# Performance work log

Hardware: AMD Instinct MI355X
Metric: run time of the kernel (lower is better)

## Reference

```python
import jax, jax.numpy as jnp
import numpy as np

B, BS, M, D = 64, 8, 512, 256  # b = bs * neg_sample_num, neg_sample_num = 8
NEG_FILL = -1e10


def setup_inputs() -> dict:
    key = jax.random.key(0)
    ks = jax.random.split(key, 7)
    x = jax.random.normal(ks[0], (B, M, D), jnp.float32)
    y = jax.random.normal(ks[1], (BS, M, D), jnp.float32)
    mask_x = jax.random.randint(ks[2], (B, M), 0, 2).astype(bool).at[:, 0].set(True)
    mask_y = jax.random.randint(ks[3], (BS, M), 0, 2).astype(bool).at[:, 0].set(True)
    scale = 1.0 / np.sqrt(D)
    Wq = jax.random.normal(ks[4], (D, D), jnp.float32) * scale  # torch Linear weight [out,in]
    Wk = jax.random.normal(ks[5], (D, D), jnp.float32) * scale
    Wv = jax.random.normal(ks[6], (D, D), jnp.float32) * scale
    return {"x": x, "y": y, "mask_x": mask_x, "mask_y": mask_y, "Wq": Wq, "Wk": Wk, "Wv": Wv}


def reference(x, y, mask_x, mask_y, Wq, Wk, Wv):
    # Projections (torch Linear: x @ W.T, no bias)
    Qx, Kx, Vx = x @ Wq.T, x @ Wk.T, x @ Wv.T
    Qy, Ky, Vy = y @ Wq.T, y @ Wk.T, y @ Wv.T
    b, m, d = Qx.shape
    bs = Ky.shape[0]
    neg = b // bs  # neg_sample_num branch (bs != b)

    scores_x = jnp.einsum('bid,bjd->bij', Qx, Kx)   # [b,m,m]
    scores_y = jnp.einsum('bid,bjd->bij', Qy, Ky)   # [bs,m,m]
    # Q_x grouped as [bs, neg, m, d] then transposed to [neg, bs, m, d];
    # K_y is tiled over neg (pure broadcast), so contract directly against [bs,m,d].
    Qx_e = Qx.reshape(bs, neg, m, d).swapaxes(0, 1)  # [neg,bs,m,d]
    scores_xy = jnp.einsum('nsid,sjd->nsij', Qx_e, Ky)  # [neg,bs,m,m]

    mx = mask_x[:, :, None]  # [b,m,1]
    my = mask_y[:, :, None]  # [bs,m,1]
    scores_x = jnp.where(mx & mx.swapaxes(1, 2), scores_x, NEG_FILL)
    scores_y = jnp.where(my & my.swapaxes(1, 2), scores_y, NEG_FILL)

    mask_xy = mask_x.reshape(bs, neg, m, 1).swapaxes(0, 1) & mask_y[None, :, None, :]  # [neg,bs,m,m]
    scores_xy = jnp.where(mask_xy, scores_xy, NEG_FILL)

    # y_len[n, s] = sum(mask_y[s]) for every n (repeat/view/sum/transpose in torch)
    y_len = jnp.broadcast_to(jnp.sum(mask_y.astype(jnp.int32), axis=1)[None, :], (neg, bs))

    probs_x = jax.nn.softmax(scores_x, axis=-1)
    probs_y = jax.nn.softmax(scores_y, axis=-1)
    probs_xy = jax.nn.softmax(scores_xy, axis=-1)

    ctx_x = jnp.einsum('bij,bjd->bid', probs_x, Vx)
    ctx_y = jnp.einsum('bij,bjd->bid', probs_y, Vy)
    return (ctx_x, ctx_y, scores_x, scores_y, probs_xy, mask_xy, y_len)
```

## Files before the change

### kernel.cpp

```cpp
#include <hip/hip_runtime.h>
#include <cstdint>

#define NEG_FILL_F (-10000000000.0f)
constexpr int BB     = 64;
constexpr int BS_    = 8;
constexpr int MM     = 512;
constexpr int DD     = 256;
constexpr int ROWS_X = BB * MM;
constexpr int ROWS_Y = BS_ * MM;
constexpr int ROWS_ALL = ROWS_X + ROWS_Y;
constexpr int K3     = 768;

typedef __attribute__((ext_vector_type(8))) short short8;
typedef __attribute__((ext_vector_type(4))) float f32x4;

__device__ inline unsigned short rne_bf16(float f) {
    unsigned int u = __float_as_uint(f);
    u = (u + 0x7FFFu + ((u >> 16) & 1u)) >> 16;
    return (unsigned short)u;
}
__device__ inline float bf2f(unsigned short h) {
    return __uint_as_float(((unsigned int)h) << 16);
}

__device__ inline f32x4 mfma16(short8 a, short8 b, f32x4 c) {
    return __builtin_amdgcn_mfma_f32_16x16x32_bf16(a, b, c, 0, 0, 0);
}

__device__ inline void gld16(const unsigned short* g, unsigned short* l) {
    __builtin_amdgcn_global_load_lds(
        (const __attribute__((address_space(1))) unsigned int*)g,
        (__attribute__((address_space(3))) unsigned int*)l, 16, 0, 0);
}

__device__ inline void mfma_4x4(const short8 af[4], const short8 bf_[4],
                                f32x4 acc[4][4]) {
    #pragma unroll
    for (int i = 0; i < 4; ++i)
        #pragma unroll
        for (int j = 0; j < 4; ++j)
            acc[i][j] = mfma16(af[i], bf_[j], acc[i][j]);
}

__device__ inline void stage768_rot(unsigned short* dstbase,
                                    const unsigned short* __restrict__ src,
                                    int ck, int wave, int lane)
{
    #pragma unroll
    for (int s = 0; s < 6; ++s) {
        const int c  = s * 256 + wave * 64 + lane;
        const int r  = c / 12;
        const int q  = c - r * 12;
        const int rm = r % 12;
        int cin = q - rm;
        cin += (cin >> 31) & 12;
        gld16(src + (size_t)r * K3 + ck * 96 + cin * 8,
              dstbase + (size_t)(s * 256 + wave * 64) * 8);
    }
}

__device__ inline void frag4_rot96(const unsigned short (*T)[96], int rbase,
                                   int lid, const int rm[4], int c0,
                                   short8 f[4])
{
    #pragma unroll
    for (int i = 0; i < 4; ++i) {
        int q = c0 + rm[i];
        if (q >= 12) q -= 12;
        f[i] = *(const short8*)&T[rbase + i * 16 + lid][q * 8];
    }
}

__global__ __launch_bounds__(256) void convw_kernel(
    const float* __restrict__ Wq, const float* __restrict__ Wk,
    const float* __restrict__ Wv, unsigned short* __restrict__ Wb)
{
    const int g  = blockIdx.x * 256 + threadIdx.x;
    const int e  = g * 8;
    const int zi = e >> 16;
    const int off = e & 65535;
    const float* W = (zi == 0) ? Wq : (zi == 1 ? Wk : Wv);
    float4 v0 = *(const float4*)(W + off);
    float4 v1 = *(const float4*)(W + off + 4);
    const float fv[8] = {v0.x, v0.y, v0.z, v0.w, v1.x, v1.y, v1.z, v1.w};
    unsigned short o[24];
    #pragma unroll
    for (int i = 0; i < 8; ++i) {
        unsigned short h = rne_bf16(fv[i]);
        unsigned short l = rne_bf16(fv[i] - bf2f(h));
        o[i*3+0] = h; o[i*3+1] = h; o[i*3+2] = l;
    }
    unsigned short* dst = Wb + (size_t)zi * 196608 + (size_t)off * 3;
    #pragma unroll
    for (int s = 0; s < 3; ++s) {
        short8 v;
        #pragma unroll
        for (int e2 = 0; e2 < 8; ++e2) v[e2] = (short)o[s*8+e2];
        *(short8*)(dst + s * 8) = v;
    }
}

__global__ __launch_bounds__(256) void convx_kernel(
    const float* __restrict__ x, const float* __restrict__ y,
    unsigned short* __restrict__ xs)
{
    const int g   = blockIdx.x * 256 + threadIdx.x;
    const int row = g >> 5;
    const int off = (g & 31) * 8;
    const float* src = (row < ROWS_X) ? (x + (size_t)row * DD)
                                      : (y + (size_t)(row - ROWS_X) * DD);
    float4 v0 = *(const float4*)(src + off);
    float4 v1 = *(const float4*)(src + off + 4);
    const float fv[8] = {v0.x, v0.y, v0.z, v0.w, v1.x, v1.y, v1.z, v1.w};
    unsigned short o[24];
    #pragma unroll
    for (int i = 0; i < 8; ++i) {
        unsigned short h = rne_bf16(fv[i]);
        unsigned short l = rne_bf16(fv[i] - bf2f(h));
        o[i*3+0] = h; o[i*3+1] = l; o[i*3+2] = h;
    }
    unsigned short* dst = xs + (size_t)row * K3 + (size_t)off * 3;
    #pragma unroll
    for (int s = 0; s < 3; ++s) {
        short8 w;
        #pragma unroll
        for (int e2 = 0; e2 < 8; ++e2) w[e2] = (short)o[s*8+e2];
        *(short8*)(dst + s * 8) = w;
    }
}

__global__ __launch_bounds__(256) void proj_kernel(
    const unsigned short* __restrict__ xs,
    const unsigned short* __restrict__ Wb,
    unsigned short* __restrict__ Qa, unsigned short* __restrict__ Kb,
    unsigned short* __restrict__ Vt,
    unsigned short* __restrict__ Qp, unsigned short* __restrict__ Kp)
{
    const int z    = blockIdx.z;
    const int row0 = blockIdx.x * 128;
    const int col0 = blockIdx.y * 128;
    const unsigned short* Asrc = xs + (size_t)row0 * K3;
    const unsigned short* Bsrc = Wb + (size_t)z * 196608 + (size_t)col0 * K3;

    __shared__ unsigned short Ab[128][96];
    __shared__ unsigned short Bb[128][96];

    const int t = threadIdx.x;
    const int wave = t >> 6, lane = t & 63, quad = lane >> 4, lid = lane & 15;
    const int wrow = (wave & 1) * 64, wcol = (wave >> 1) * 64;

    int rma[4], rmb[4];
    #pragma unroll
    for (int i = 0; i < 4; ++i) {
        rma[i] = (wrow + i * 16 + lid) % 12;
        rmb[i] = (wcol + i * 16 + lid) % 12;
    }

    f32x4 acc[4][4];
    #pragma unroll
    for (int i = 0; i < 4; ++i)
        #pragma unroll
        for (int j = 0; j < 4; ++j) acc[i][j] = (f32x4){0.f, 0.f, 0.f, 0.f};

    for (int ck = 0; ck < 8; ++ck) {
        stage768_rot(&Ab[0][0], Asrc, ck, wave, lane);
        stage768_rot(&Bb[0][0], Bsrc, ck, wave, lane);
        __syncthreads();
        #pragma unroll
        for (int kk = 0; kk < 96; kk += 32) {
            const int c0 = (kk >> 3) + quad;
            short8 af[4], bf_[4];
            frag4_rot96(Ab, wrow, lid, rma, c0, af);
            frag4_rot96(Bb, wcol, lid, rmb, c0, bf_);
            mfma_4x4(af, bf_, acc);
        }
        __syncthreads();
    }

    if (z == 2) {
        #pragma unroll
        for (int i = 0; i < 4; ++i) {
            const int rg = row0 + wrow + i * 16 + quad * 4;
            const int b  = rg >> 9;
            const int j  = rg & 511;
            #pragma unroll
            for (int jt = 0; jt < 4; ++jt) {
                const int col = col0 + wcol + jt * 16 + lid;
                *(ushort4*)(Vt + (size_t)b * DD * MM + (size_t)col * MM + j) =
                    make_ushort4(rne_bf16(acc[i][jt][0]), rne_bf16(acc[i][jt][1]),
                                 rne_bf16(acc[i][jt][2]), rne_bf16(acc[i][jt][3]));
            }
        }
    } else {
        unsigned short* dst = (z == 0) ? Qa : Kb;
        const bool aform = (z == 0);
        unsigned short* plain = nullptr;
        int rbase_plain = 0;
        if (z == 0 && row0 < ROWS_X) { plain = Qp; rbase_plain = 0; }
        if (z == 1 && row0 >= ROWS_X) { plain = Kp; rbase_plain = ROWS_X; }
        #pragma unroll
        for (int i = 0; i < 4; ++i) {
            const int rg = row0 + wrow + i * 16 + quad * 4;
            #pragma unroll
            for (int r = 0; r < 4; ++r) {
                unsigned short* rowp = dst + (size_t)(rg + r) * K3;
                unsigned short* prow = plain
                    ? (plain + (size_t)(rg + r - rbase_plain) * DD) : nullptr;
                #pragma unroll
                for (int jt = 0; jt < 4; ++jt) {
                    const int col = col0 + wcol + jt * 16 + lid;
                    const float v = acc[i][jt][r];
                    unsigned short h = rne_bf16(v);
                    unsigned short l = rne_bf16(v - bf2f(h));
                    rowp[3*col+0] = h;
                    rowp[3*col+1] = aform ? l : h;
                    rowp[3*col+2] = aform ? h : l;
                    if (prow) prow[col] = h;
                }
            }
        }
    }
}

__global__ __launch_bounds__(256) void scores_self_kernel(
    const unsigned short* __restrict__ Qa,
    const unsigned short* __restrict__ Kb,
    const int* __restrict__ mask_x, const int* __restrict__ mask_y,
    float* __restrict__ Sbase, float2* __restrict__ pstats)
{
    const int z    = blockIdx.z;
    const int row0 = blockIdx.x * 128;
    const int col0 = blockIdx.y * 128;
    const unsigned short* Asrc = Qa + (size_t)(z * MM + row0) * K3;
    const unsigned short* Bsrc = Kb + (size_t)(z * MM + col0) * K3;
    const int* msk = (z < 64) ? (mask_x + z * MM) : (mask_y + (z - 64) * MM);
    float* S = Sbase + (size_t)z * MM * MM;

    __shared__ unsigned short Ab[128][96];
    __shared__ unsigned short Bb[128][96];
    __shared__ float pm2[128][2];
    __shared__ float ps2[128][2];

    const int t = threadIdx.x;
    const int wave = t >> 6, lane = t & 63, quad = lane >> 4, lid = lane & 15;
    const int wrow = (wave & 1) * 64, wcol = (wave >> 1) * 64;

    int rma[4], rmb[4];
    #pragma unroll
    for (int i = 0; i < 4; ++i) {
        rma[i] = (wrow + i * 16 + lid) % 12;
        rmb[i] = (wcol + i * 16 + lid) % 12;
    }

    f32x4 acc[4][4];
    #pragma unroll
    for (int i = 0; i < 4; ++i)
        #pragma unroll
        for (int j = 0; j < 4; ++j) acc[i][j] = (f32x4){0.f, 0.f, 0.f, 0.f};

    for (int ck = 0; ck < 8; ++ck) {
        stage768_rot(&Ab[0][0], Asrc, ck, wave, lane);
        stage768_rot(&Bb[0][0], Bsrc, ck, wave, lane);
        __syncthreads();
        #pragma unroll
        for (int kk = 0; kk < 96; kk += 32) {
            const int c0 = (kk >> 3) + quad;
            short8 af[4], bf_[4];
            frag4_rot96(Ab, wrow, lid, rma, c0, af);
            frag4_rot96(Bb, wcol, lid, rmb, c0, bf_);
            mfma_4x4(af, bf_, acc);
        }
        __syncthreads();
    }

    int mcol[4];
    #pragma unroll
    for (int jt = 0; jt < 4; ++jt) mcol[jt] = msk[col0 + wcol + jt * 16 + lid];

    #pragma unroll
    for (int i = 0; i < 4; ++i) {
        const int rl0 = wrow + i * 16 + quad * 4;
        #pragma unroll
        for (int r = 0; r < 4; ++r) {
            const int rlocal = rl0 + r;
            const int rg = row0 + rlocal;
            const bool mr = (msk[rg] != 0);
            float* Srow = S + (size_t)rg * MM;
            float v[4];
            float mt = -3.4e38f;
            #pragma unroll
            for (int jt = 0; jt < 4; ++jt) {
                const int col = col0 + wcol + jt * 16 + lid;
                const bool valid = mr && (mcol[jt] != 0);
                v[jt] = valid ? acc[i][jt][r] : NEG_FILL_F;
                Srow[col] = v[jt];
                mt = fmaxf(mt, v[jt]);
            }
            #pragma unroll
            for (int o = 1; o < 16; o <<= 1) mt = fmaxf(mt, __shfl_xor(mt, o));
            float se = 0.f;
            #pragma unroll
            for (int jt = 0; jt < 4; ++jt) se += __expf(v[jt] - mt);
            #pragma unroll
            for (int o = 1; o < 16; o <<= 1) se += __shfl_xor(se, o);
            if (lid == 0) { pm2[rlocal][wave >> 1] = mt; ps2[rlocal][wave >> 1] = se; }
        }
    }
    __syncthreads();
    if (t < 128) {
        const float m0 = pm2[t][0], m1 = pm2[t][1];
        const float mm = fmaxf(m0, m1);
        const float ss = ps2[t][0] * __expf(m0 - mm) + ps2[t][1] * __expf(m1 - mm);
        pstats[(size_t)(z * 4 + blockIdx.y) * MM + row0 + t] = make_float2(mm, ss);
    }
}

__global__ __launch_bounds__(256) void scores_xy_kernel(
    const unsigned short* __restrict__ Qp, const unsigned short* __restrict__ Kp,
    const int* __restrict__ mask_x, const int* __restrict__ mask_y,
    float* __restrict__ Sbase, float* __restrict__ Mbase,
    float2* __restrict__ pstats)
{
    const int z = blockIdx.z;
    const int n = z >> 3, s = z & 7;
    const int bq = s * 8 + n;
    const int bk = s;
    const int row0 = blockIdx.x * 128;
    const int col0 = blockIdx.y * 128;
    const unsigned short* Asrc = Qp + (size_t)(bq * MM + row0) * DD;
    const unsigned short* Bsrc = Kp + (size_t)(bk * MM + col0) * DD;
    const int* mq = mask_x + bq * MM;
    const int* mk = mask_y + bk * MM;
    float* Sl = Sbase + (size_t)z * MM * MM;
    float* Ml = Mbase + (size_t)z * MM * MM;

    __shared__ unsigned short Ab[128][64];
    __shared__ unsigned short Bb[128][64];
    __shared__ float pm2[128][2];
    __shared__ float ps2[128][2];

    const int t = threadIdx.x;
    const int wave = t >> 6, lane = t & 63, quad = lane >> 4, lid = lane & 15;
    const int wrow = (wave & 1) * 64, wcol = (wave >> 1) * 64;
    const int x7 = lid & 7;

    f32x4 acc[4][4];
    #pragma unroll
    for (int i = 0; i < 4; ++i)
        #pragma unroll
        for (int j = 0; j < 4; ++j) acc[i][j] = (f32x4){0.f, 0.f, 0.f, 0.f};

    for (int ck = 0; ck < 4; ++ck) {
        #pragma unroll
        for (int s4 = 0; s4 < 4; ++s4) {
            const int c   = s4 * 256 + wave * 64 + lane;
            const int r   = c >> 3;
            const int cin = (c & 7) ^ (r & 7);
            gld16(Asrc + (size_t)r * DD + ck * 64 + cin * 8,
                  &Ab[0][0] + (size_t)(s4 * 256 + wave * 64) * 8);
        }
        #pragma unroll
        for (int s4 = 0; s4 < 4; ++s4) {
            const int c   = s4 * 256 + wave * 64 + lane;
            const int r   = c >> 3;
            const int cin = (c & 7) ^ (r & 7);
            gld16(Bsrc + (size_t)r * DD + ck * 64 + cin * 8,
                  &Bb[0][0] + (size_t)(s4 * 256 + wave * 64) * 8);
        }
        __syncthreads();
        #pragma unroll
        for (int kk = 0; kk < 64; kk += 32) {
            const int c0 = (kk >> 3) + quad;
            const int q  = c0 ^ x7;
            short8 af[4], bf_[4];
            #pragma unroll
            for (int i = 0; i < 4; ++i) {
                af[i]  = *(const short8*)&Ab[wrow + i * 16 + lid][q * 8];
                bf_[i] = *(const short8*)&Bb[wcol + i * 16 + lid][q * 8];
            }
            mfma_4x4(af, bf_, acc);
        }
        __syncthreads();
    }

    int mcol[4];
    #pragma unroll
    for (int jt = 0; jt < 4; ++jt) mcol[jt] = mk[col0 + wcol + jt * 16 + lid];

    #pragma unroll
    for (int i = 0; i < 4; ++i) {
        const int rl0 = wrow + i * 16 + quad * 4;
        #pragma unroll
        for (int r = 0; r < 4; ++r) {
            const int rlocal = rl0 + r;
            const int rg = row0 + rlocal;
            const bool mr = (mq[rg] != 0);
            float* Srow = Sl + (size_t)rg * MM;
            float* Mrow = Ml + (size_t)rg * MM;
            float v[4];
            float mt = -3.4e38f;
            #pragma unroll
            for (int jt = 0; jt < 4; ++jt) {
                const int col = col0 + wcol + jt * 16 + lid;
                const bool valid = mr && (mcol[jt] != 0);
                v[jt] = valid ? acc[i][jt][r] : NEG_FILL_F;
                Srow[col] = v[jt];
                Mrow[col] = valid ? 1.0f : 0.0f;
                mt = fmaxf(mt, v[jt]);
            }
            #pragma unroll
            for (int o = 1; o < 16; o <<= 1) mt = fmaxf(mt, __shfl_xor(mt, o));
            float se = 0.f;
            #pragma unroll
            for (int jt = 0; jt < 4; ++jt) se += __expf(v[jt] - mt);
            #pragma unroll
            for (int o = 1; o < 16; o <<= 1) se += __shfl_xor(se, o);
            if (lid == 0) { pm2[rlocal][wave >> 1] = mt; ps2[rlocal][wave >> 1] = se; }
        }
    }
    __syncthreads();
    if (t < 128) {
        const float m0 = pm2[t][0], m1 = pm2[t][1];
        const float mm = fmaxf(m0, m1);
        const float ss = ps2[t][0] * __expf(m0 - mm) + ps2[t][1] * __expf(m1 - mm);
        pstats[(size_t)(z * 4 + blockIdx.y) * MM + row0 + t] = make_float2(mm, ss);
    }
}

__global__ __launch_bounds__(256) void reduce4_kernel(
    const float2* __restrict__ p, float2* __restrict__ st)
{
    const int row = blockIdx.x * 256 + threadIdx.x;
    const int z = row >> 9, rl = row & 511;
    float m = -3.4e38f, s = 0.f;
    #pragma unroll
    for (int by = 0; by < 4; ++by) {
        float2 v = p[(size_t)(z * 4 + by) * MM + rl];
        float nm = fmaxf(m, v.x);
        s = s * __expf(m - nm) + v.y * __expf(v.x - nm);
        m = nm;
    }
    st[row] = make_float2(m, 1.0f / s);
}

__global__ __launch_bounds__(256) void ctx_kernel(
    const float* __restrict__ Sbase, const float2* __restrict__ stats,
    const unsigned short* __restrict__ Vt_base, float* __restrict__ Obase)
{
    const int b = blockIdx.z;
    const float*          S  = Sbase + (size_t)b * MM * MM;
    const float2*         st = stats + (size_t)b * MM;
    const unsigned short* Vt = Vt_base + (size_t)b * DD * MM;
    float*                O  = Obase + (size_t)b * MM * DD;

    const int row0 = blockIdx.x * 128;
    const int col0 = blockIdx.y * 128;

    __shared__ unsigned short Ab[128][72];
    __shared__ unsigned short Bb[128][64];

    const int t = threadIdx.x;
    const int wave = t >> 6, lane = t & 63, quad = lane >> 4, lid = lane & 15;
    const int wrow = (wave & 1) * 64, wcol = (wave >> 1) * 64;
    const int x7 = lid & 7;

    f32x4 acc[4][4];
    #pragma unroll
    for (int i = 0; i < 4; ++i)
        #pragma unroll
        for (int j = 0; j < 4; ++j) acc[i][j] = (f32x4){0.f, 0.f, 0.f, 0.f};

    for (int ck = 0; ck < 8; ++ck) {
        #pragma unroll
        for (int s4 = 0; s4 < 4; ++s4) {
            const int c   = s4 * 256 + wave * 64 + lane;
            const int r   = c >> 3;
            const int cin = (c & 7) ^ (r & 7);
            gld16(Vt + (size_t)(col0 + r) * MM + ck * 64 + cin * 8,
                  &Bb[0][0] + (size_t)(s4 * 256 + wave * 64) * 8);
        }
        #pragma unroll
        for (int s4 = 0; s4 < 4; ++s4) {
            const int c   = s4 * 256 + t;
            const int row = c >> 3;
            const int j8  = (c & 7) * 8;
            const float* sp = S + (size_t)(row0 + row) * MM + ck * 64 + j8;
            float4 v0 = *(const float4*)sp;
            float4 v1 = *(const float4*)(sp + 4);
            const float pm = st[row0 + row].x;
            short8 pk;
            pk[0] = (short)rne_bf16(__expf(v0.x - pm));
            pk[1] = (short)rne_bf16(__expf(v0.y - pm));
            pk[2] = (short)rne_bf16(__expf(v0.z - pm));
            pk[3] = (short)rne_bf16(__expf(v0.w - pm));
            pk[4] = (short)rne_bf16(__expf(v1.x - pm));
            pk[5] = (short)rne_bf16(__expf(v1.y - pm));
            pk[6] = (short)rne_bf16(__expf(v1.z - pm));
            pk[7] = (short)rne_bf16(__expf(v1.w - pm));
            *(short8*)&Ab[row][j8] = pk;
        }
        __syncthreads();
        #pragma unroll
        for (int kk = 0; kk < 64; kk += 32) {
            const int c0 = (kk >> 3) + quad;
            const int q  = c0 ^ x7;
            short8 af[4], bf_[4];
            #pragma unroll
            for (int i = 0; i < 4; ++i) {
                af[i]  = *(const short8*)&Ab[wrow + i * 16 + lid][kk + quad * 8];
                bf_[i] = *(const short8*)&Bb[wcol + i * 16 + lid][q * 8];
            }
            mfma_4x4(af, bf_, acc);
        }
        __syncthreads();
    }

    #pragma unroll
    for (int i = 0; i < 4; ++i) {
        const int rgb = row0 + wrow + i * 16 + quad * 4;
        float inv[4];
        #pragma unroll
        for (int r = 0; r < 4; ++r) inv[r] = st[rgb + r].y;
        #pragma unroll
        for (int jt = 0; jt < 4; ++jt) {
            const int col = col0 + wcol + jt * 16 + lid;
            #pragma unroll
            for (int r = 0; r < 4; ++r)
                O[(size_t)(rgb + r) * DD + col] = acc[i][jt][r] * inv[r];
        }
    }
}

__global__ __launch_bounds__(128) void softmax_apply(
    float* __restrict__ S, const float2* __restrict__ stats)
{
    const int row = blockIdx.x;
    const float2 st = stats[row];
    float4* r = (float4*)(S + (size_t)row * MM) + threadIdx.x;
    float4 v = *r;
    v.x = __expf(v.x - st.x) * st.y;
    v.y = __expf(v.y - st.x) * st.y;
    v.z = __expf(v.z - st.x) * st.y;
    v.w = __expf(v.w - st.x) * st.y;
    *r = v;
}

__global__ void ylen_kernel(const int* __restrict__ mask_y, float* __restrict__ out)
{
    const int s = blockIdx.x;
    const int lane = threadIdx.x;
    int c = 0;
    #pragma unroll
    for (int k = 0; k < 8; ++k) c += (mask_y[s * MM + k * 64 + lane] != 0);
    #pragma unroll
    for (int off = 32; off; off >>= 1) c += __shfl_xor(c, off);
    if (lane < 8) out[lane * 8 + s] = (float)c;
}

extern "C" void kernel_launch(void* const* d_in, const int* in_sizes, int n_in,
                              void* d_out, int out_size, void* d_ws, size_t ws_size,
                              hipStream_t stream)
{
    const float* x      = (const float*)d_in[0];
    const float* y      = (const float*)d_in[1];
    const int*   mask_x = (const int*)d_in[2];
    const int*   mask_y = (const int*)d_in[3];
    const float* Wq     = (const float*)d_in[4];
    const float* Wk     = (const float*)d_in[5];
    const float* Wv     = (const float*)d_in[6];
    float* out = (float*)d_out;

    unsigned short* Wb = (unsigned short*)d_ws;
    unsigned short* Qa = Wb + 589824;
    unsigned short* Kb = Qa + 28311552;
    unsigned short* Vt = Kb + 28311552;
    float2* stats_x  = (float2*)(Vt + 9437184);
    float2* stats_xy = stats_x + ROWS_ALL;
    float2* ps_x  = stats_x + (ROWS_ALL + ROWS_X);
    float2* ps_xy = ps_x + (64 + 8) * 4 * 512;

    float* out_ctx_x = out;
    float* out_sx    = out + 9437184;
    float* out_pxy   = out + 28311552;
    float* out_mxy   = out + 45088768;
    float* out_ylen  = out + 61865984;

    unsigned short* xs = (unsigned short*)out_pxy;
    unsigned short* Qp = (unsigned short*)out_ctx_x;
    unsigned short* Kp = Qp + (size_t)ROWS_X * DD;

    convw_kernel<<<96, 256, 0, stream>>>(Wq, Wk, Wv, Wb);
    convx_kernel<<<4608, 256, 0, stream>>>(x, y, xs);

    proj_kernel<<<dim3(288, 2, 3), 256, 0, stream>>>(xs, Wb, Qa, Kb, Vt, Qp, Kp);

    scores_self_kernel<<<dim3(4, 4, 72), 256, 0, stream>>>(
        Qa, Kb, mask_x, mask_y, out_sx, ps_x);
    scores_xy_kernel<<<dim3(4, 4, 64), 256, 0, stream>>>(
        Qp, Kp, mask_x, mask_y, out_pxy, out_mxy, ps_xy);

    reduce4_kernel<<<(ROWS_ALL + ROWS_X) / 256, 256, 0, stream>>>(ps_x, stats_x);

    ctx_kernel<<<dim3(4, 2, 72), 256, 0, stream>>>(out_sx, stats_x, Vt, out_ctx_x);

    softmax_apply<<<ROWS_X, 128, 0, stream>>>(out_pxy, stats_xy);

    ylen_kernel<<<8, 64, 0, stream>>>(mask_y, out_ylen);
}
```

Measured before the change: 552.4 us.

## Store Q/K as hi|lo planes, fuse input conversion into projection, drop plain copies

Replaces the interleaved 3-way split-bf16 layout (K=768) with a planar hi/lo layout (K=512 storage), so the emulated 3-term product reads hi/lo slices by offset rather than storing duplicated halves. This cuts the Q/K workspace footprint and write traffic. The x/y bf16 split conversion is fused into the projection's A-tile staging, and the separate convx kernel is removed. Plain Q/K copies for the cross scores are dropped because that kernel now reads the hi plane of Qa/Kb directly. The ctx A-tile gets an XOR swizzle instead of padding, and a few launches are reordered; the risk is extra fp32 global loads and conversion work inside the projection loop.

Measured after the change: 567.6 us. +2.8%, slower.

```diff
diff --git a/kernel.cpp b/kernel.cpp
--- a/kernel.cpp
+++ b/kernel.cpp
@@ -9,7 +9,7 @@
 constexpr int ROWS_X = BB * MM;
 constexpr int ROWS_Y = BS_ * MM;
 constexpr int ROWS_ALL = ROWS_X + ROWS_Y;
-constexpr int K3     = 768;
+constexpr int KS     = 512;
 
 typedef __attribute__((ext_vector_type(8))) short short8;
 typedef __attribute__((ext_vector_type(4))) float f32x4;
@@ -42,9 +42,10 @@
             acc[i][j] = mfma16(af[i], bf_[j], acc[i][j]);
 }
 
-__device__ inline void stage768_rot(unsigned short* dstbase,
-                                    const unsigned short* __restrict__ src,
-                                    int ck, int wave, int lane)
+template<bool ASIDE>
+__device__ inline void stage_qk(unsigned short* dstbase,
+                                const unsigned short* __restrict__ src,
+                                int ck, int wave, int lane)
 {
     #pragma unroll
     for (int s = 0; s < 6; ++s) {
@@ -54,7 +55,12 @@
         const int rm = r % 12;
         int cin = q - rm;
         cin += (cin >> 31) & 12;
-        gld16(src + (size_t)r * K3 + ck * 96 + cin * 8,
+        const int slotb = ck * 96 + cin * 8;
+        const int p  = slotb >> 8;
+        const int c8 = slotb & 255;
+        const int off = ASIDE ? ((p == 1) ? 256 : 0)
+                              : ((p == 2) ? 256 : 0);
+        gld16(src + (size_t)r * KS + off + c8,
               dstbase + (size_t)(s * 256 + wave * 64) * 8);
     }
 }
@@ -79,68 +85,35 @@
     const int e  = g * 8;
     const int zi = e >> 16;
     const int off = e & 65535;
+    const int row = off >> 8, k0 = off & 255;
     const float* W = (zi == 0) ? Wq : (zi == 1 ? Wk : Wv);
     float4 v0 = *(const float4*)(W + off);
     float4 v1 = *(const float4*)(W + off + 4);
     const float fv[8] = {v0.x, v0.y, v0.z, v0.w, v1.x, v1.y, v1.z, v1.w};
-    unsigned short o[24];
+    short8 hh, ll;
     #pragma unroll
     for (int i = 0; i < 8; ++i) {
         unsigned short h = rne_bf16(fv[i]);
-        unsigned short l = rne_bf16(fv[i] - bf2f(h));
-        o[i*3+0] = h; o[i*3+1] = h; o[i*3+2] = l;
-    }
-    unsigned short* dst = Wb + (size_t)zi * 196608 + (size_t)off * 3;
-    #pragma unroll
-    for (int s = 0; s < 3; ++s) {
-        short8 v;
-        #pragma unroll
-        for (int e2 = 0; e2 < 8; ++e2) v[e2] = (short)o[s*8+e2];
-        *(short8*)(dst + s * 8) = v;
-    }
-}
-
-__global__ __launch_bounds__(256) void convx_kernel(
+        hh[i] = (short)h;
+        ll[i] = (short)rne_bf16(fv[i] - bf2f(h));
+    }
+    unsigned short* dst = Wb + (size_t)zi * 131072 + (size_t)row * KS;
+    *(short8*)(dst + k0)       = hh;
+    *(short8*)(dst + 256 + k0) = ll;
+}
+
+__global__ __launch_bounds__(256) void proj_kernel(
     const float* __restrict__ x, const float* __restrict__ y,
-    unsigned short* __restrict__ xs)
-{
-    const int g   = blockIdx.x * 256 + threadIdx.x;
-    const int row = g >> 5;
-    const int off = (g & 31) * 8;
-    const float* src = (row < ROWS_X) ? (x + (size_t)row * DD)
-                                      : (y + (size_t)(row - ROWS_X) * DD);
-    float4 v0 = *(const float4*)(src + off);
-    float4 v1 = *(const float4*)(src + off + 4);
-    const float fv[8] = {v0.x, v0.y, v0.z, v0.w, v1.x, v1.y, v1.z, v1.w};
-    unsigned short o[24];
-    #pragma unroll
-    for (int i = 0; i < 8; ++i) {
-        unsigned short h = rne_bf16(fv[i]);
-        unsigned short l = rne_bf16(fv[i] - bf2f(h));
-        o[i*3+0] = h; o[i*3+1] = l; o[i*3+2] = h;
-    }
-    unsigned short* dst = xs + (size_t)row * K3 + (size_t)off * 3;
-    #pragma unroll
-    for (int s = 0; s < 3; ++s) {
-        short8 w;
-        #pragma unroll
-        for (int e2 = 0; e2 < 8; ++e2) w[e2] = (short)o[s*8+e2];
-        *(short8*)(dst + s * 8) = w;
-    }
-}
-
-__global__ __launch_bounds__(256) void proj_kernel(
-    const unsigned short* __restrict__ xs,
     const unsigned short* __restrict__ Wb,
     unsigned short* __restrict__ Qa, unsigned short* __restrict__ Kb,
-    unsigned short* __restrict__ Vt,
-    unsigned short* __restrict__ Qp, unsigned short* __restrict__ Kp)
+    unsigned short* __restrict__ Vt)
 {
     const int z    = blockIdx.z;
     const int row0 = blockIdx.x * 128;
     const int col0 = blockIdx.y * 128;
-    const unsigned short* Asrc = xs + (size_t)row0 * K3;
-    const unsigned short* Bsrc = Wb + (size_t)z * 196608 + (size_t)col0 * K3;
+    const float* A = (row0 < ROWS_X) ? (x + (size_t)row0 * DD)
+                                     : (y + (size_t)(row0 - ROWS_X) * DD);
+    const unsigned short* Bsrc = Wb + (size_t)z * 131072 + (size_t)col0 * KS;
 
     __shared__ unsigned short Ab[128][96];
     __shared__ unsigned short Bb[128][96];
@@ -163,8 +136,35 @@
         for (int j = 0; j < 4; ++j) acc[i][j] = (f32x4){0.f, 0.f, 0.f, 0.f};
 
     for (int ck = 0; ck < 8; ++ck) {
-        stage768_rot(&Ab[0][0], Asrc, ck, wave, lane);
-        stage768_rot(&Bb[0][0], Bsrc, ck, wave, lane);
+        stage_qk<false>(&Bb[0][0], Bsrc, ck, wave, lane);
+        #pragma unroll
+        for (int s = 0; s < 6; ++s) {
+            const int c  = s * 256 + t;
+            const int r  = c / 12;
+            const int q  = c - r * 12;
+            const int rm = r % 12;
+            int cin = q - rm;
+            cin += (cin >> 31) & 12;
+            const int slotb = ck * 96 + cin * 8;
+            const int p  = slotb >> 8;
+            const int c8 = slotb & 255;
+            const float* ap = A + (size_t)r * DD + c8;
+            float4 v0 = *(const float4*)ap;
+            float4 v1 = *(const float4*)(ap + 4);
+            const float fv[8] = {v0.x, v0.y, v0.z, v0.w, v1.x, v1.y, v1.z, v1.w};
+            short8 o;
+            if (p == 1) {
+                #pragma unroll
+                for (int e = 0; e < 8; ++e) {
+                    unsigned short h = rne_bf16(fv[e]);
+                    o[e] = (short)rne_bf16(fv[e] - bf2f(h));
+                }
+            } else {
+                #pragma unroll
+                for (int e = 0; e < 8; ++e) o[e] = (short)rne_bf16(fv[e]);
+            }
+            *(short8*)&Ab[r][q * 8] = o;
+        }
         __syncthreads();
         #pragma unroll
         for (int kk = 0; kk < 96; kk += 32) {
@@ -193,29 +193,19 @@
         }
     } else {
         unsigned short* dst = (z == 0) ? Qa : Kb;
-        const bool aform = (z == 0);
-        unsigned short* plain = nullptr;
-        int rbase_plain = 0;
-        if (z == 0 && row0 < ROWS_X) { plain = Qp; rbase_plain = 0; }
-        if (z == 1 && row0 >= ROWS_X) { plain = Kp; rbase_plain = ROWS_X; }
         #pragma unroll
         for (int i = 0; i < 4; ++i) {
             const int rg = row0 + wrow + i * 16 + quad * 4;
             #pragma unroll
             for (int r = 0; r < 4; ++r) {
-                unsigned short* rowp = dst + (size_t)(rg + r) * K3;
-                unsigned short* prow = plain
-                    ? (plain + (size_t)(rg + r - rbase_plain) * DD) : nullptr;
+                unsigned short* rowp = dst + (size_t)(rg + r) * KS;
                 #pragma unroll
                 for (int jt = 0; jt < 4; ++jt) {
                     const int col = col0 + wcol + jt * 16 + lid;
                     const float v = acc[i][jt][r];
                     unsigned short h = rne_bf16(v);
-                    unsigned short l = rne_bf16(v - bf2f(h));
-                    rowp[3*col+0] = h;
-                    rowp[3*col+1] = aform ? l : h;
-                    rowp[3*col+2] = aform ? h : l;
-                    if (prow) prow[col] = h;
+                    rowp[col]       = h;
+                    rowp[256 + col] = rne_bf16(v - bf2f(h));
                 }
             }
         }
@@ -231,8 +221,8 @@
     const int z    = blockIdx.z;
     const int row0 = blockIdx.x * 128;
     const int col0 = blockIdx.y * 128;
-    const unsigned short* Asrc = Qa + (size_t)(z * MM + row0) * K3;
-    const unsigned short* Bsrc = Kb + (size_t)(z * MM + col0) * K3;
+    const unsigned short* Asrc = Qa + (size_t)(z * MM + row0) * KS;
+    const unsigned short* Bsrc = Kb + (size_t)(z * MM + col0) * KS;
     const int* msk = (z < 64) ? (mask_x + z * MM) : (mask_y + (z - 64) * MM);
     float* S = Sbase + (size_t)z * MM * MM;
 
@@ -259,8 +249,8 @@
         for (int j = 0; j < 4; ++j) acc[i][j] = (f32x4){0.f, 0.f, 0.f, 0.f};
 
     for (int ck = 0; ck < 8; ++ck) {
-        stage768_rot(&Ab[0][0], Asrc, ck, wave, lane);
-        stage768_rot(&Bb[0][0], Bsrc, ck, wave, lane);
+        stage_qk<true >(&Ab[0][0], Asrc, ck, wave, lane);
+        stage_qk<false>(&Bb[0][0], Bsrc, ck, wave, lane);
         __syncthreads();
         #pragma unroll
         for (int kk = 0; kk < 96; kk += 32) {
@@ -316,7 +306,7 @@
 }
 
 __global__ __launch_bounds__(256) void scores_xy_kernel(
-    const unsigned short* __restrict__ Qp, const unsigned short* __restrict__ Kp,
+    const unsigned short* __restrict__ Qa, const unsigned short* __restrict__ Kb,
     const int* __restrict__ mask_x, const int* __restrict__ mask_y,
     float* __restrict__ Sbase, float* __restrict__ Mbase,
     float2* __restrict__ pstats)
@@ -327,8 +317,8 @@
     const int bk = s;
     const int row0 = blockIdx.x * 128;
     const int col0 = blockIdx.y * 128;
-    const unsigned short* Asrc = Qp + (size_t)(bq * MM + row0) * DD;
-    const unsigned short* Bsrc = Kp + (size_t)(bk * MM + col0) * DD;
+    const unsigned short* Asrc = Qa + (size_t)(bq * MM + row0) * KS;
+    const unsigned short* Bsrc = Kb + (size_t)((ROWS_X + bk * MM) + col0) * KS;
     const int* mq = mask_x + bq * MM;
     const int* mk = mask_y + bk * MM;
     float* Sl = Sbase + (size_t)z * MM * MM;
@@ -356,7 +346,7 @@
             const int c   = s4 * 256 + wave * 64 + lane;
             const int r   = c >> 3;
             const int cin = (c & 7) ^ (r & 7);
-            gld16(Asrc + (size_t)r * DD + ck * 64 + cin * 8,
+            gld16(Asrc + (size_t)r * KS + ck * 64 + cin * 8,
                   &Ab[0][0] + (size_t)(s4 * 256 + wave * 64) * 8);
         }
         #pragma unroll
@@ -364,7 +354,7 @@
             const int c   = s4 * 256 + wave * 64 + lane;
             const int r   = c >> 3;
             const int cin = (c & 7) ^ (r & 7);
-            gld16(Bsrc + (size_t)r * DD + ck * 64 + cin * 8,
+            gld16(Bsrc + (size_t)r * KS + ck * 64 + cin * 8,
                   &Bb[0][0] + (size_t)(s4 * 256 + wave * 64) * 8);
         }
         __syncthreads();
@@ -456,7 +446,7 @@
     const int row0 = blockIdx.x * 128;
     const int col0 = blockIdx.y * 128;
 
-    __shared__ unsigned short Ab[128][72];
+    __shared__ unsigned short Ab[128][64];
     __shared__ unsigned short Bb[128][64];
 
     const int t = threadIdx.x;
@@ -481,9 +471,10 @@
         }
         #pragma unroll
         for (int s4 = 0; s4 < 4; ++s4) {
-            const int c   = s4 * 256 + t;
-            const int row = c >> 3;
-            const int j8  = (c & 7) * 8;
+            const int c    = s4 * 256 + t;
+            const int row  = c >> 3;
+            const int j8   = (c & 7) * 8;
+            const int slot = (c & 7) ^ (row & 7);
             const float* sp = S + (size_t)(row0 + row) * MM + ck * 64 + j8;
             float4 v0 = *(const float4*)sp;
             float4 v1 = *(const float4*)(sp + 4);
@@ -497,7 +488,7 @@
             pk[5] = (short)rne_bf16(__expf(v1.y - pm));
             pk[6] = (short)rne_bf16(__expf(v1.z - pm));
             pk[7] = (short)rne_bf16(__expf(v1.w - pm));
-            *(short8*)&Ab[row][j8] = pk;
+            *(short8*)&Ab[row][slot * 8] = pk;
         }
         __syncthreads();
         #pragma unroll
@@ -507,7 +498,7 @@
             short8 af[4], bf_[4];
             #pragma unroll
             for (int i = 0; i < 4; ++i) {
-                af[i]  = *(const short8*)&Ab[wrow + i * 16 + lid][kk + quad * 8];
+                af[i]  = *(const short8*)&Ab[wrow + i * 16 + lid][q * 8];
                 bf_[i] = *(const short8*)&Bb[wcol + i * 16 + lid][q * 8];
             }
             mfma_4x4(af, bf_, acc);
@@ -571,9 +562,9 @@
     float* out = (float*)d_out;
 
     unsigned short* Wb = (unsigned short*)d_ws;
-    unsigned short* Qa = Wb + 589824;
-    unsigned short* Kb = Qa + 28311552;
-    unsigned short* Vt = Kb + 28311552;
+    unsigned short* Qa = Wb + 393216;
+    unsigned short* Kb = Qa + 18874368;
+    unsigned short* Vt = Kb + 18874368;
     float2* stats_x  = (float2*)(Vt + 9437184);
     float2* stats_xy = stats_x + ROWS_ALL;
     float2* ps_x  = stats_x + (ROWS_ALL + ROWS_X);
@@ -585,25 +576,19 @@
     float* out_mxy   = out + 45088768;
     float* out_ylen  = out + 61865984;
 
-    unsigned short* xs = (unsigned short*)out_pxy;
-    unsigned short* Qp = (unsigned short*)out_ctx_x;
-    unsigned short* Kp = Qp + (size_t)ROWS_X * DD;
-
     convw_kernel<<<96, 256, 0, stream>>>(Wq, Wk, Wv, Wb);
-    convx_kernel<<<4608, 256, 0, stream>>>(x, y, xs);
-
-    proj_kernel<<<dim3(288, 2, 3), 256, 0, stream>>>(xs, Wb, Qa, Kb, Vt, Qp, Kp);
+    ylen_kernel<<<8, 64, 0, stream>>>(mask_y, out_ylen);
+
+    proj_kernel<<<dim3(288, 2, 3), 256, 0, stream>>>(x, y, Wb, Qa, Kb, Vt);
 
     scores_self_kernel<<<dim3(4, 4, 72), 256, 0, stream>>>(
         Qa, Kb, mask_x, mask_y, out_sx, ps_x);
     scores_xy_kernel<<<dim3(4, 4, 64), 256, 0, stream>>>(
-        Qp, Kp, mask_x, mask_y, out_pxy, out_mxy, ps_xy);
+        Qa, Kb, mask_x, mask_y, out_pxy, out_mxy, ps_xy);
 
     reduce4_kernel<<<(ROWS_ALL + ROWS_X) / 256, 256, 0, stream>>>(ps_x, stats_x);
 
+    softmax_apply<<<ROWS_X, 128, 0, stream>>>(out_pxy, stats_xy);
+
     ctx_kernel<<<dim3(4, 2, 72), 256, 0, stream>>>(out_sx, stats_x, Vt, out_ctx_x);
-
-    softmax_apply<<<ROWS_X, 128, 0, stream>>>(out_pxy, stats_xy);
-
-    ylen_kernel<<<8, 64, 0, stream>>>(mask_y, out_ylen);
-}
+}
```
